# Optimization experiments

Hardware: AMD Instinct MI355X
Metric: run time of the kernel (lower is better)

The kernel has to match this reference:

```python
import jax, jax.numpy as jnp
import numpy as np

NEG = jnp.float32(-1e30)  # log-space -inf surrogate (safe for grads)


def _ctc_neg_log_likelihood(logprobs, labels, input_lens, label_lens):
    """CTC forward (alpha) recursion, blank=0.
    logprobs: (T, N, V) log-softmax outputs; labels: (N, L) int; lens: (N,).
    Returns per-sample negative log-likelihood (N,).
    """
    T, N, V = logprobs.shape
    L = labels.shape[1]
    S = 2 * L + 1
    # Extended label sequence: blank, l1, blank, l2, ..., blank
    z = jnp.zeros((N, S), dtype=labels.dtype).at[:, 1::2].set(labels)
    # Per-step emission log-probs for extended labels: (T, N, S)
    lp = logprobs[:, jnp.arange(N)[:, None], z]
    # Skip connection s-2 -> s allowed iff z[s] != blank and z[s] != z[s-2]
    z_m2 = jnp.pad(z, ((0, 0), (2, 0)))[:, :S]
    skip = (z != 0) & (z != z_m2)
    skip = skip.at[:, :2].set(False)

    alpha0 = jnp.full((N, S), NEG, dtype=logprobs.dtype)
    alpha0 = alpha0.at[:, 0].set(lp[0, :, 0]).at[:, 1].set(lp[0, :, 1])

    def step(alpha, xs):
        lp_t, t = xs
        a1 = jnp.pad(alpha, ((0, 0), (1, 0)), constant_values=NEG)[:, :S]
        a2 = jnp.pad(alpha, ((0, 0), (2, 0)), constant_values=NEG)[:, :S]
        a2 = jnp.where(skip, a2, NEG)
        new = jnp.logaddexp(jnp.logaddexp(alpha, a1), a2) + lp_t
        # Freeze alpha once past each sample's input length
        new = jnp.where((t < input_lens)[:, None], new, alpha)
        return new, None

    ts = jnp.arange(1, T)
    alpha, _ = jax.lax.scan(step, alpha0, (lp[1:], ts))

    idx_blank = (2 * label_lens).astype(jnp.int32)  # final blank position
    end1 = jnp.take_along_axis(alpha, idx_blank[:, None], axis=1)[:, 0]
    end2 = jnp.take_along_axis(alpha, (idx_blank - 1)[:, None], axis=1)[:, 0]
    return -jnp.logaddexp(end1, end2)


def setup_inputs() -> dict:
    key = jax.random.key(0)
    k1, k2, k3, k4, k5 = jax.random.split(key, 5)
    N, T, D, V, L = 16, 512, 512, 4096, 128
    encoder_out = jax.random.normal(k1, (N, T, D), dtype=jnp.float32)
    W = jax.random.normal(k2, (D, V), dtype=jnp.float32) / jnp.sqrt(jnp.float32(D))
    b = jnp.zeros((V,), dtype=jnp.float32)
    encoder_out_lens = jax.random.randint(k3, (N,), 300, T + 1, dtype=jnp.int32)
    padded_labels = jax.random.randint(k4, (N, L), 1, V, dtype=jnp.int32)
    label_lengths = jax.random.randint(k5, (N,), 64, L + 1, dtype=jnp.int32)
    return {
        "encoder_out": encoder_out,
        "W": W,
        "b": b,
        "encoder_out_lens": encoder_out_lens,
        "padded_labels": padded_labels,
        "label_lengths": label_lengths,
    }


def reference(encoder_out, W, b, encoder_out_lens, padded_labels, label_lengths):
    # Dropout is identity in eval mode. proj -> (N, T, V)
    logits = jnp.einsum("ntd,dv->ntv", encoder_out, W) + b
    # transpose(0,1).log_softmax(2) -> (T, N, V)
    logprobs = jax.nn.log_softmax(logits.transpose(1, 0, 2), axis=2)
    nll = _ctc_neg_log_likelihood(logprobs, padded_labels, encoder_out_lens, label_lengths)
    # reduction='sum', then divided by batch size
    return jnp.sum(nll) / padded_labels.shape[0]
```

## Files before the change

### kernel.cpp

```cpp
#include <hip/hip_runtime.h>

#define NEGF (-1e30f)
#define LOG2E 1.4426950408889634f
#define LN2d  0.6931471805599453

typedef __attribute__((ext_vector_type(8))) short bf16x8;
typedef __attribute__((ext_vector_type(4))) float f32x4;

__device__ __forceinline__ unsigned short f2bf(float x) {
  unsigned u = __float_as_uint(x);
  unsigned r = (u + 0x7FFFu + ((u >> 16) & 1u)) >> 16;
  return (unsigned short)r;
}


__device__ __forceinline__ void d_cvtx(int bid, int tid,
                                       const float* __restrict__ X,
                                       unsigned short* __restrict__ Xbf) {
  const int i = bid * 256 + tid;
  float4 v = ((const float4*)X)[i];
  ushort4 h;
  h.x = f2bf(v.x); h.y = f2bf(v.y); h.z = f2bf(v.z); h.w = f2bf(v.w);
  ((ushort4*)Xbf)[i] = h;
}

__device__ __forceinline__ void d_gather(int bid, int tid,
                                         const float* __restrict__ W,
                                         const float* __restrict__ b,
                                         const int* __restrict__ labels,
                                         float* __restrict__ Wgt,
                                         float* __restrict__ gb) {
  const int n  = bid >> 7;
  const int kc = bid & 127;
  const int k0 = kc << 2;
  for (int idx = tid; idx < 4 * 129; idx += 256) {
    const int kk = idx / 129;
    const int j  = idx - kk * 129;
    const int c  = (j == 0) ? 0 : labels[n * 128 + (j - 1)];
    const int k  = k0 + kk;
    Wgt[((size_t)(n * 512 + k)) * 132 + j] = W[(size_t)k * 4096 + c];
    if (kc == 0 && kk == 0) gb[n * 129 + j] = b[c];
  }
}

__device__ __forceinline__ void d_glp_raw(int bid, int tid, char* smem,
                                          const float* __restrict__ X,
                                          const float* __restrict__ Wgt,
                                          const float* __restrict__ gb,
                                          const int* __restrict__ lens,
                                          float* __restrict__ g) {
  const int n  = bid >> 4;
  const int t0 = (bid & 15) << 5;
  if (t0 >= lens[n]) return;
  const int m0 = n * 512 + t0;
  float (*xs)[512] = (float (*)[512])smem;
  {
    const float4* Xv = (const float4*)(X + (size_t)m0 * 512);
    float4* xsv = (float4*)(&xs[0][0]);
    for (int i = tid; i < 32 * 128; i += 256) xsv[i] = Xv[i];
  }
  __syncthreads();
  const int j = tid;
  if (j >= 129) return;
  const float* wp = Wgt + (size_t)(n * 512) * 132 + j;
  float acc[32];
#pragma unroll
  for (int r = 0; r < 32; ++r) acc[r] = 0.f;
  float w0 = wp[0], w1 = wp[132], w2 = wp[264], w3 = wp[396];
  for (int k4 = 0; k4 < 128; ++k4) {
    const int kn = (k4 + 1) & 127;
    float p0 = wp[(size_t)(kn * 4 + 0) * 132];
    float p1 = wp[(size_t)(kn * 4 + 1) * 132];
    float p2 = wp[(size_t)(kn * 4 + 2) * 132];
    float p3 = wp[(size_t)(kn * 4 + 3) * 132];
#pragma unroll
    for (int r = 0; r < 32; ++r) {
      float4 x4 = *(const float4*)(&xs[r][k4 << 2]);
      acc[r] = fmaf(x4.x, w0, acc[r]);
      acc[r] = fmaf(x4.y, w1, acc[r]);
      acc[r] = fmaf(x4.z, w2, acc[r]);
      acc[r] = fmaf(x4.w, w3, acc[r]);
    }
    w0 = p0; w1 = p1; w2 = p2; w3 = p3;
  }
  const float bb = gb[n * 129 + j];
#pragma unroll
  for (int r = 0; r < 32; ++r)
    g[(size_t)(m0 + r) * 132 + j] = (acc[r] + bb) * LOG2E;
}

__device__ __forceinline__ void d_wtrans(int bid, int tid, char* smem,
                                         const float* __restrict__ W,
                                         unsigned short* __restrict__ Wt) {
  float (*tile)[65] = (float (*)[65])smem;
  const int kb = bid & 7;
  const int vb = bid >> 3;
  const int k0 = kb << 6, v0 = vb << 6;
#pragma unroll
  for (int it = 0; it < 16; ++it) {
    const int idx = it * 256 + tid;
    const int r = idx >> 6, c = idx & 63;
    tile[r][c] = W[(size_t)(k0 + r) * 4096 + v0 + c];
  }
  __syncthreads();
#pragma unroll
  for (int it = 0; it < 16; ++it) {
    const int idx = it * 256 + tid;
    const int vr = idx >> 6, kc = idx & 63;
    Wt[(size_t)(v0 + vr) * 512 + k0 + kc] = f2bf(tile[kc][vr]);
  }
}

__device__ __forceinline__ void stage_tile(const unsigned short* __restrict__ src,
                                           int r0, char* ldsbase, int wave,
                                           int tid, int kbyte) {
#pragma unroll
  for (int j = 0; j < 2; ++j) {
    const int chunk = (tid & 3) ^ ((tid >> 3) & 3);
    const char* gp = (const char*)src +
        (size_t)(r0 + j * 64 + (tid >> 2)) * 1024 + kbyte + chunk * 16;
    char* lp = ldsbase + j * 4096 + wave * 1024;
    __builtin_amdgcn_global_load_lds(
        (const __attribute__((address_space(1))) unsigned int*)gp,
        (__attribute__((address_space(3))) unsigned int*)lp, 16, 0, 0);
  }
}

__device__ __forceinline__ void d_gemm(int gid, int tid, char* smem,
                                       const unsigned short* __restrict__ Xbf,
                                       const unsigned short* __restrict__ Wt,
                                       const float* __restrict__ bvec,
                                       const int* __restrict__ lens,
                                       float* __restrict__ pg) {
  const int bm = gid >> 5;
  const int bn = gid & 31;
  const int n  = bm >> 2;
  const int t0 = (bm & 3) << 7;
  if (t0 >= lens[n]) return;
  const int m0 = bm << 7;
  const int v0 = bn << 7;

  const int wave = tid >> 6;
  const int lane = tid & 63;
  const int lrow = lane & 15;
  const int lk   = (lane >> 4) * 16;
  const int lks  = lk ^ (((lrow >> 1) & 3) << 4);
  const int wr   = wave >> 1;
  const int wn   = wave & 1;

  f32x4 acc[4][4];
#pragma unroll
  for (int mi = 0; mi < 4; ++mi)
#pragma unroll
    for (int ni = 0; ni < 4; ++ni) acc[mi][ni] = (f32x4){0.f, 0.f, 0.f, 0.f};

  {
    char* buf = smem;
    stage_tile(Xbf, m0, buf + 0,    wave, tid, 0);
    stage_tile(Wt,  v0, buf + 8192, wave, tid, 0);
  }
  __syncthreads();

  int cur = 0;
  for (int kk = 0; kk < 16; ++kk) {
    if (kk < 15) {
      char* nbuf = smem + (cur ^ 1) * 16384;
      const int kb = (kk + 1) << 6;
      stage_tile(Xbf, m0, nbuf + 0,    wave, tid, kb);
      stage_tile(Wt,  v0, nbuf + 8192, wave, tid, kb);
    }
    const char* buf = smem + cur * 16384;
    bf16x8 ah[4], bh[4];
#pragma unroll
    for (int mi = 0; mi < 4; ++mi) {
      const int off = (wr * 64 + mi * 16 + lrow) * 64 + lks;
      ah[mi] = *(const bf16x8*)(buf + off);
    }
#pragma unroll
    for (int ni = 0; ni < 4; ++ni) {
      const int off = (wn * 64 + ni * 16 + lrow) * 64 + lks;
      bh[ni] = *(const bf16x8*)(buf + 8192 + off);
    }
#pragma unroll
    for (int mi = 0; mi < 4; ++mi)
#pragma unroll
      for (int ni = 0; ni < 4; ++ni)
        acc[mi][ni] = __builtin_amdgcn_mfma_f32_16x16x32_bf16(ah[mi], bh[ni], acc[mi][ni], 0, 0, 0);
    __syncthreads();
    cur ^= 1;
  }

  const float lg2e = LOG2E;
  float bias[4];
#pragma unroll
  for (int ni = 0; ni < 4; ++ni) bias[ni] = bvec[v0 + wn * 64 + ni * 16 + lrow];
  float* part = (float*)(smem + 32768);
#pragma unroll
  for (int mi = 0; mi < 4; ++mi)
#pragma unroll
    for (int reg = 0; reg < 4; ++reg) {
      float s = 0.f;
#pragma unroll
      for (int ni = 0; ni < 4; ++ni)
        s += exp2f((acc[mi][ni][reg] + bias[ni]) * lg2e);
#pragma unroll
      for (int msk = 1; msk < 16; msk <<= 1) s += __shfl_xor(s, msk);
      if (lrow == 0)
        part[(wr * 64 + mi * 16 + (lane >> 4) * 4 + reg) * 2 + wn] = s;
    }
  __syncthreads();
  if (tid < 128)
    pg[(size_t)(m0 + tid) * 32 + bn] = part[tid * 2 + 0] + part[tid * 2 + 1];
}

__device__ __forceinline__ float lae32(float x, float y, float z) {
  float m = fmaxf(fmaxf(x, y), z);
  float e = exp2f(x - m) + exp2f(y - m) + exp2f(z - m);
  return m + __log2f(e);
}

__device__ __forceinline__ float lae3n(float x, float y, float z) {
  float m = fmaxf(fmaxf(x, y), z);
  float e = __expf(x - m) + __expf(y - m) + __expf(z - m);
  return m + __logf(e);
}

__device__ __forceinline__ void stage32(const float* __restrict__ gsrc,
                                        char* ldsbase, int tid, int wave) {
#pragma unroll
  for (int k = 0; k < 4; ++k) {
    const char* gp = (const char*)gsrc + k * 4096 + (size_t)tid * 16;
    char* lp = ldsbase + k * 4096 + wave * 1024;
    __builtin_amdgcn_global_load_lds(
        (const __attribute__((address_space(1))) unsigned int*)gp,
        (__attribute__((address_space(3))) unsigned int*)lp, 16, 0, 0);
  }
  if (tid < 32) {
    const char* gp = (const char*)gsrc + 16384 + (size_t)tid * 16;
    char* lp = ldsbase + 16384;
    __builtin_amdgcn_global_load_lds(
        (const __attribute__((address_space(1))) unsigned int*)gp,
        (__attribute__((address_space(3))) unsigned int*)lp, 16, 0, 0);
  }
}

__device__ void d_scan(int sbid, int tid, char* smem,
                       const float* __restrict__ g,
                       const int* __restrict__ labels,
                       const int* __restrict__ in_lens,
                       const int* __restrict__ lab_lens,
                       float* __restrict__ af,
                       float* __restrict__ ab) {
  const int n    = sbid >> 1;
  const int dir  = sbid & 1;
  const int wave = tid >> 6;
  const int l    = tid & 63;
  const int len  = in_lens[n];
  const int tm   = len >> 1;
  const float* gn = g + (size_t)n * 512 * 132;
  const int s0 = 5 * l;

  int jm0, jm1, jm2, jm3, jm4;
  {
    int jmv[5];
#pragma unroll
    for (int i = 0; i < 5; ++i) {
      const int s = s0 + i;
      jmv[i] = (s < 257 && (s & 1)) ? ((s + 1) >> 1) : 0;
    }
    jm0 = jmv[0]; jm1 = jmv[1]; jm2 = jmv[2]; jm3 = jmv[3]; jm4 = jmv[4];
  }

  if (dir == 0) {
    bool sk0, sk1, sk2, sk3, sk4;
    {
      bool skv[5];
#pragma unroll
      for (int i = 0; i < 5; ++i) {
        const int s = s0 + i;
        skv[i] = false;
        if (s < 257 && (s & 1) && s >= 3) {
          const int li = (s - 1) >> 1;
          const int cl = labels[n * 128 + li];
          skv[i] = (cl != 0) && (cl != labels[n * 128 + li - 1]);
        }
      }
      sk0 = skv[0]; sk1 = skv[1]; sk2 = skv[2]; sk3 = skv[3]; sk4 = skv[4];
    }
    stage32(gn, smem, tid, wave);
    __syncthreads();

    float a0 = NEGF, a1 = NEGF, a2 = NEGF, a3 = NEGF, a4 = NEGF;
    if (tid < 64 && l == 0) {
      const float* B0 = (const float*)smem;
      a0 = B0[0]; a1 = B0[1];
    }
    float a3p = NEGF, a4p = NEGF;

    int t = 1, c = 0;
    while (true) {
      const bool more = ((c + 1) << 5) <= tm;
      if (more)
        stage32(gn + (size_t)((c + 1) << 5) * 132,
                smem + ((c + 1) & 1) * 16896, tid, wave);
      if (tid < 64) {
        const float* B = (const float*)(smem + (c & 1) * 16896);
        const int ce = (c << 5) + 31;
        const int tend = (tm < ce) ? tm : ce;
        int ro = (t - (c << 5)) * 132;
        float p0 = B[ro + jm0], p1 = B[ro + jm1], p2 = B[ro + jm2],
              p3 = B[ro + jm3], p4 = B[ro + jm4];
        for (; t <= tend; ++t) {
          const int ro2 = (t < tend) ? ro + 132 : ro;
          const float q0 = B[ro2 + jm0];
          const float q1 = B[ro2 + jm1];
          const float q2 = B[ro2 + jm2];
          const float q3 = B[ro2 + jm3];
          const float q4 = B[ro2 + jm4];
          float x3 = a3p, x4 = a4p;
          if (l == 0) { x3 = NEGF; x4 = NEGF; }
          const float n3 = lae32(a3, a2, sk3 ? a1 : NEGF) + p3;
          const float n4 = lae32(a4, a3, sk4 ? a2 : NEGF) + p4;
          a3p = __shfl_up(n3, 1);
          a4p = __shfl_up(n4, 1);
          const float n0 = lae32(a0, x4, sk0 ? x3 : NEGF) + p0;
          const float n1 = lae32(a1, a0, sk1 ? x4 : NEGF) + p1;
          const float n2 = lae32(a2, a1, sk2 ? a0 : NEGF) + p2;
          a0 = n0; a1 = n1; a2 = n2; a3 = n3; a4 = n4;
          p0 = q0; p1 = q1; p2 = q2; p3 = q3; p4 = q4;
          ro = ro2;
        }
      }
      if (!more) break;
      __syncthreads();
      ++c;
    }
    if (tid < 64) {
      float* o = af + n * 320 + s0;
      o[0] = a0; o[1] = a1; o[2] = a2; o[3] = a3; o[4] = a4;
    }
  } else {
    bool skd0, skd1, skd2, skd3, skd4;
    {
      bool skv[5];
#pragma unroll
      for (int i = 0; i < 5; ++i) {
        const int s2 = s0 + i + 2;
        skv[i] = false;
        if (s2 < 257 && (s2 & 1) && s2 >= 3) {
          const int li = (s2 - 1) >> 1;
          const int cl = labels[n * 128 + li];
          skv[i] = (cl != 0) && (cl != labels[n * 128 + li - 1]);
        }
      }
      skd0 = skv[0]; skd1 = skv[1]; skd2 = skv[2]; skd3 = skv[3]; skd4 = skv[4];
    }
    int c = (len - 1) >> 5;
    stage32(gn + (size_t)(c << 5) * 132, smem + (c & 1) * 16896, tid, wave);
    __syncthreads();

    float b0, b1, b2, b3, b4;
    {
      const int ll = lab_lens[n];
      const int i1 = 2 * ll, i2 = 2 * ll - 1;
      b0 = (s0 + 0 == i1 || s0 + 0 == i2) ? 0.f : NEGF;
      b1 = (s0 + 1 == i1 || s0 + 1 == i2) ? 0.f : NEGF;
      b2 = (s0 + 2 == i1 || s0 + 2 == i2) ? 0.f : NEGF;
      b3 = (s0 + 3 == i1 || s0 + 3 == i2) ? 0.f : NEGF;
      b4 = (s0 + 4 == i1 || s0 + 4 == i2) ? 0.f : NEGF;
    }

    int t = len - 2;
    while (true) {
      const bool more = (c << 5) > tm + 1;
      if (more)
        stage32(gn + (size_t)((c - 1) << 5) * 132,
                smem + ((c - 1) & 1) * 16896, tid, wave);
      if (tid < 64) {
        const float* B = (const float*)(smem + (c & 1) * 16896);
        const int cl0 = (c << 5) - 1;
        const int tlo = (tm > cl0) ? tm : cl0;
        int ro = (t + 1 - (c << 5)) * 132;
        float p0 = B[ro + jm0], p1 = B[ro + jm1], p2 = B[ro + jm2],
              p3 = B[ro + jm3], p4 = B[ro + jm4];
        for (; t >= tlo; --t) {
          const int ro2 = (t - 1 >= tlo) ? ro - 132 : ro;
          const float q0 = B[ro2 + jm0];
          const float q1 = B[ro2 + jm1];
          const float q2 = B[ro2 + jm2];
          const float q3 = B[ro2 + jm3];
          const float q4 = B[ro2 + jm4];
          const float c0 = b0 + p0;
          const float c1 = b1 + p1;
          float c5 = __shfl_down(c0, 1);
          float c6 = __shfl_down(c1, 1);
          const float c2 = b2 + p2;
          const float c3 = b3 + p3;
          const float c4 = b4 + p4;
          const float m0n = lae32(c0, c1, skd0 ? c2 : NEGF);
          const float m1n = lae32(c1, c2, skd1 ? c3 : NEGF);
          const float m2n = lae32(c2, c3, skd2 ? c4 : NEGF);
          if (l == 63) { c5 = NEGF; c6 = NEGF; }
          const float m3n = lae32(c3, c4, skd3 ? c5 : NEGF);
          const float m4n = lae32(c4, c5, skd4 ? c6 : NEGF);
          b0 = m0n; b1 = m1n; b2 = m2n; b3 = m3n; b4 = m4n;
          p0 = q0; p1 = q1; p2 = q2; p3 = q3; p4 = q4;
          ro = ro2;
        }
      }
      if (!more) break;
      __syncthreads();
      --c;
    }
    if (tid < 64) {
      float* o = ab + n * 320 + s0;
      o[0] = b0; o[1] = b1; o[2] = b2; o[3] = b3; o[4] = b4;
    }
  }
}


__global__ __launch_bounds__(256) void k_prep1(const float* __restrict__ X,
                                               unsigned short* __restrict__ Xbf,
                                               const float* __restrict__ W,
                                               const float* __restrict__ b,
                                               const int* __restrict__ labels,
                                               float* __restrict__ Wgt,
                                               float* __restrict__ gb) {
  const int bid = blockIdx.x;
  if (bid < 4096) d_cvtx(bid, threadIdx.x, X, Xbf);
  else            d_gather(bid - 4096, threadIdx.x, W, b, labels, Wgt, gb);
}

__global__ __launch_bounds__(256) void k_prep2(const float* __restrict__ X,
                                               const float* __restrict__ Wgt,
                                               const float* __restrict__ gb,
                                               const int* __restrict__ lens,
                                               float* __restrict__ g,
                                               const float* __restrict__ W,
                                               unsigned short* __restrict__ Wt) {
  __shared__ __align__(16) char smem[65536];
  const int bid = blockIdx.x;
  if (bid < 256) d_glp_raw(bid, threadIdx.x, smem, X, Wgt, gb, lens, g);
  else           d_wtrans(bid - 256, threadIdx.x, smem, W, Wt);
}

__global__ __launch_bounds__(256, 4) void k_main(const float* __restrict__ g,
                                                 const int* __restrict__ labels,
                                                 const int* __restrict__ in_lens,
                                                 const int* __restrict__ lab_lens,
                                                 float* __restrict__ af,
                                                 float* __restrict__ ab,
                                                 const unsigned short* __restrict__ Xbf,
                                                 const unsigned short* __restrict__ Wt,
                                                 const float* __restrict__ bvec,
                                                 float* __restrict__ pg) {
  __shared__ __align__(16) char smem[33792];
  const int bid = blockIdx.x;
  if (bid < 32) {
    __builtin_amdgcn_s_setprio(1);
    d_scan(bid, threadIdx.x, smem, g, labels, in_lens, lab_lens, af, ab);
    __builtin_amdgcn_s_setprio(0);
  } else {
    d_gemm(bid - 32, threadIdx.x, smem, Xbf, Wt, bvec, in_lens, pg);
  }
}

__global__ __launch_bounds__(256) void k_tail(const float* __restrict__ pg,
                                              const int* __restrict__ lens,
                                              const float* __restrict__ af,
                                              const float* __restrict__ ab,
                                              float* __restrict__ nll) {
  const int n = blockIdx.x, tid = threadIdx.x;
  const int len = lens[n];
  __shared__ double red[256];
  double s = 0.0;
  for (int t = tid; t < len; t += 256) {
    const float4* p = (const float4*)(pg + ((size_t)(n * 512 + t)) * 32);
    float e = 0.f;
#pragma unroll
    for (int i = 0; i < 8; ++i) { float4 v = p[i]; e += v.x + v.y + v.z + v.w; }
    s += (double)__logf(e);
  }
  red[tid] = s;
  __syncthreads();
  for (int off = 128; off > 0; off >>= 1) {
    if (tid < off) red[tid] += red[tid + off];
    __syncthreads();
  }
  if (tid < 64) {
    const int l = tid;
    const int s0 = 5 * l;
    float v0 = NEGF, v1 = NEGF, v2 = NEGF, v3 = NEGF, v4 = NEGF;
    const float* f = af + n * 320 + s0;
    const float* bb = ab + n * 320 + s0;
    if (s0 + 0 < 257) v0 = f[0] + bb[0];
    if (s0 + 1 < 257) v1 = f[1] + bb[1];
    if (s0 + 2 < 257) v2 = f[2] + bb[2];
    if (s0 + 3 < 257) v3 = f[3] + bb[3];
    if (s0 + 4 < 257) v4 = f[4] + bb[4];
    float M = fmaxf(fmaxf(v0, v1), fmaxf(fmaxf(v2, v3), v4));
#pragma unroll
    for (int off = 1; off < 64; off <<= 1) M = fmaxf(M, __shfl_xor(M, off));
    float e = exp2f(v0 - M) + exp2f(v1 - M) + exp2f(v2 - M)
            + exp2f(v3 - M) + exp2f(v4 - M);
#pragma unroll
    for (int off = 1; off < 64; off <<= 1) e += __shfl_xor(e, off);
    if (l == 0)
      nll[n] = (float)(red[0] - (double)(M + __log2f(e)) * LN2d);
  }
}

__global__ void k_finish(const float* __restrict__ nll, float* __restrict__ out) {
  const int l = threadIdx.x;
  float v = (l < 16) ? nll[l] : 0.f;
#pragma unroll
  for (int off = 8; off > 0; off >>= 1) v += __shfl_down(v, off);
  if (l == 0) out[0] = v * 0.0625f;
}

__global__ void k_gather_w(const float* __restrict__ W,
                           const float* __restrict__ b,
                           const int* __restrict__ labels,
                           float* __restrict__ Wgt,
                           float* __restrict__ gb) {
  d_gather(blockIdx.x, threadIdx.x, W, b, labels, Wgt, gb);
}

__global__ __launch_bounds__(256) void k_glp(const float* __restrict__ X,
                                             const float* __restrict__ Wgt,
                                             const float* __restrict__ gb,
                                             const float* __restrict__ lse,
                                             const int* __restrict__ lens,
                                             float* __restrict__ g) {
  const int blk = blockIdx.x;
  const int n   = blk >> 4;
  const int t0  = (blk & 15) << 5;
  if (t0 >= lens[n]) return;
  const int m0 = n * 512 + t0;
  __shared__ float xs[32][512];
  {
    const float4* Xv = (const float4*)(X + (size_t)m0 * 512);
    float4* xsv = (float4*)(&xs[0][0]);
    for (int i = threadIdx.x; i < 32 * 128; i += 256) xsv[i] = Xv[i];
  }
  __syncthreads();
  const int j = threadIdx.x;
  if (j >= 129) return;
  const float* wp = Wgt + (size_t)(n * 512) * 132 + j;
  float acc[32];
#pragma unroll
  for (int r = 0; r < 32; ++r) acc[r] = 0.f;
  float w0 = wp[0], w1 = wp[132], w2 = wp[264], w3 = wp[396];
  for (int k4 = 0; k4 < 128; ++k4) {
    const int kn = (k4 + 1) & 127;
    float p0 = wp[(size_t)(kn * 4 + 0) * 132];
    float p1 = wp[(size_t)(kn * 4 + 1) * 132];
    float p2 = wp[(size_t)(kn * 4 + 2) * 132];
    float p3 = wp[(size_t)(kn * 4 + 3) * 132];
#pragma unroll
    for (int r = 0; r < 32; ++r) {
      float4 x4 = *(const float4*)(&xs[r][k4 << 2]);
      acc[r] = fmaf(x4.x, w0, acc[r]);
      acc[r] = fmaf(x4.y, w1, acc[r]);
      acc[r] = fmaf(x4.z, w2, acc[r]);
      acc[r] = fmaf(x4.w, w3, acc[r]);
    }
    w0 = p0; w1 = p1; w2 = p2; w3 = p3;
  }
  const float bb = gb[n * 129 + j];
#pragma unroll
  for (int r = 0; r < 32; ++r)
    g[(size_t)(m0 + r) * 132 + j] = acc[r] + bb - lse[m0 + r];
}

__global__ void k_ctc_g(const float* __restrict__ g,
                        const int* __restrict__ labels,
                        const int* __restrict__ in_lens,
                        const int* __restrict__ lab_lens,
                        float* __restrict__ nll) {
  const int n = blockIdx.x;
  const int l = threadIdx.x;
  const float* gn = g + (size_t)n * 512 * 132;
  const int len = in_lens[n];
  const int s0 = 5 * l;
  int jm[5]; bool sk[5];
#pragma unroll
  for (int i = 0; i < 5; ++i) {
    const int s = s0 + i;
    const bool valid = (s < 257);
    jm[i] = (valid && (s & 1)) ? ((s + 1) >> 1) : 0;
    sk[i] = false;
    if (valid && (s & 1) && s >= 3) {
      const int li = (s - 1) >> 1;
      const int cl = labels[n * 128 + li];
      sk[i] = (cl != 0) && (cl != labels[n * 128 + li - 1]);
    }
  }
  float a[5];
  a[0] = (l == 0) ? gn[0] : NEGF;
  a[1] = (l == 0) ? gn[1] : NEGF;
  a[2] = NEGF; a[3] = NEGF; a[4] = NEGF;
  float lp[5];
#pragma unroll
  for (int i = 0; i < 5; ++i) lp[i] = gn[132 + jm[i]];
  for (int t = 1; t < len; ++t) {
    const int tp = (t + 1 < len) ? (t + 1) : t;
    float np[5];
#pragma unroll
    for (int i = 0; i < 5; ++i) np[i] = gn[(size_t)tp * 132 + jm[i]];
    float a3p = __shfl_up(a[3], 1);
    float a4p = __shfl_up(a[4], 1);
    if (l == 0) { a3p = NEGF; a4p = NEGF; }
    const float b0 = lae3n(a[0], a4p,  sk[0] ? a3p  : NEGF) + lp[0];
    const float b1 = lae3n(a[1], a[0], sk[1] ? a4p  : NEGF) + lp[1];
    const float b2 = lae3n(a[2], a[1], sk[2] ? a[0] : NEGF) + lp[2];
    const float b3 = lae3n(a[3], a[2], sk[3] ? a[1] : NEGF) + lp[3];
    const float b4 = lae3n(a[4], a[3], sk[4] ? a[2] : NEGF) + lp[4];
    a[0] = b0; a[1] = b1; a[2] = b2; a[3] = b3; a[4] = b4;
#pragma unroll
    for (int i = 0; i < 5; ++i) lp[i] = np[i];
  }
  __shared__ float al[320];
#pragma unroll
  for (int i = 0; i < 5; ++i) al[s0 + i] = a[i];
  __syncthreads();
  if (l == 0) {
    const int ll  = lab_lens[n];
    const int idx = 2 * ll;
    const float e1 = al[idx], e2 = al[idx - 1];
    const float m = fmaxf(e1, e2);
    const float r = m + __logf(__expf(e1 - m) + __expf(e2 - m));
    nll[n] = -r;
  }
}

__global__ __launch_bounds__(512, 2) void k_lse(const float* __restrict__ X,
                                                const float* __restrict__ W,
                                                const float* __restrict__ b,
                                                const int* __restrict__ lens,
                                                float* __restrict__ lse,
                                                float* __restrict__ red_g) {
  const int blk = blockIdx.x;
  const int n   = blk >> 4;
  const int t0  = (blk & 15) << 5;
  if (t0 >= lens[n]) return;
  const int m0 = n * 512 + t0;
  __shared__ float xs[32][512];
  {
    const float4* Xv = (const float4*)(X + (size_t)m0 * 512);
    float4* xsv = (float4*)(&xs[0][0]);
    for (int i = threadIdx.x; i < 32 * 128; i += 512) xsv[i] = Xv[i];
  }
  float* redb = red_g + (size_t)blk * 256;
  for (int i = threadIdx.x; i < 256; i += 512) redb[i] = 0.f;
  __syncthreads();
  const int wave = threadIdx.x >> 6;
  const int lane = threadIdx.x & 63;
  for (int j = 0; j < 4; ++j) {
    const int v = (j << 10) + (threadIdx.x << 1);
    const float* Wv = W + v;
    float2 acc[32];
#pragma unroll
    for (int r = 0; r < 32; ++r) acc[r] = make_float2(0.f, 0.f);
    float2 w0 = *(const float2*)(Wv + 0 * 4096);
    float2 w1 = *(const float2*)(Wv + 1 * 4096);
    float2 w2 = *(const float2*)(Wv + 2 * 4096);
    float2 w3 = *(const float2*)(Wv + 3 * 4096);
    for (int k4 = 0; k4 < 128; ++k4) {
      const int kn = (k4 + 1) & 127;
      float2 p0 = *(const float2*)(Wv + (kn * 4 + 0) * 4096);
      float2 p1 = *(const float2*)(Wv + (kn * 4 + 1) * 4096);
      float2 p2 = *(const float2*)(Wv + (kn * 4 + 2) * 4096);
      float2 p3 = *(const float2*)(Wv + (kn * 4 + 3) * 4096);
#pragma unroll
      for (int r = 0; r < 32; ++r) {
        float4 x4 = *(const float4*)(&xs[r][k4 << 2]);
        acc[r].x = fmaf(x4.x, w0.x, acc[r].x);
        acc[r].y = fmaf(x4.x, w0.y, acc[r].y);
        acc[r].x = fmaf(x4.y, w1.x, acc[r].x);
        acc[r].y = fmaf(x4.y, w1.y, acc[r].y);
        acc[r].x = fmaf(x4.z, w2.x, acc[r].x);
        acc[r].y = fmaf(x4.z, w2.y, acc[r].y);
        acc[r].x = fmaf(x4.w, w3.x, acc[r].x);
        acc[r].y = fmaf(x4.w, w3.y, acc[r].y);
      }
      w0 = p0; w1 = p1; w2 = p2; w3 = p3;
    }
    const float2 bb = *(const float2*)(b + v);
#pragma unroll
    for (int r = 0; r < 32; ++r) {
      float e = __expf(acc[r].x + bb.x) + __expf(acc[r].y + bb.y);
#pragma unroll
      for (int off = 32; off > 0; off >>= 1) e += __shfl_xor(e, off);
      if (lane == 0) redb[wave * 32 + r] += e;
    }
  }
  __syncthreads();
  if (threadIdx.x < 32) {
    float s = 0.f;
#pragma unroll
    for (int w = 0; w < 8; ++w) s += redb[w * 32 + threadIdx.x];
    lse[m0 + threadIdx.x] = __logf(s);
  }
}

extern "C" void kernel_launch(void* const* d_in, const int* in_sizes, int n_in,
                              void* d_out, int out_size, void* d_ws, size_t ws_size,
                              hipStream_t stream) {
  const float* X        = (const float*)d_in[0];
  const float* W        = (const float*)d_in[1];
  const float* b        = (const float*)d_in[2];
  const int*   in_lens  = (const int*)d_in[3];
  const int*   labels   = (const int*)d_in[4];
  const int*   lab_lens = (const int*)d_in[5];
  float* out = (float*)d_out;
  char* wsb = (char*)d_ws;

  const size_t NEED = 34906240;
  if (ws_size >= NEED) {
    float* pg  = (float*)(wsb + 32768);
    float* Wgt = (float*)(wsb + 1081344);
    float* gb  = (float*)(wsb + 5406720);
    float* g   = (float*)(wsb + 5414976);
    float* nll = (float*)(wsb + 9740352);
    unsigned short* Xbf = (unsigned short*)(wsb + 9740416);
    unsigned short* Wt  = (unsigned short*)(wsb + 18129024);
    float* af = (float*)(wsb + 26517632);
    float* ab = (float*)(wsb + 26517632 + 20480);

    k_prep1<<<dim3(6144), dim3(256), 0, stream>>>(X, Xbf, W, b, labels, Wgt, gb);
    k_prep2<<<dim3(768), dim3(256), 0, stream>>>(X, Wgt, gb, in_lens, g, W, Wt);
    k_main<<<dim3(2080), dim3(256), 0, stream>>>(g, labels, in_lens, lab_lens,
                                                 af, ab, Xbf, Wt, b, pg);
    k_tail<<<dim3(16), dim3(256), 0, stream>>>(pg, in_lens, af, ab, nll);
    k_finish<<<dim3(1), dim3(64), 0, stream>>>(nll, out);
  } else {
    float* ws    = (float*)d_ws;
    float* lse   = ws;
    float* red_g = ws + 8192;
    float* Wgt   = ws + 8192 + 65536;
    float* gb    = Wgt + 1081344;
    float* g     = gb + 2064;
    float* nll   = g + 1081344;
    k_lse<<<dim3(256), dim3(512), 0, stream>>>(X, W, b, in_lens, lse, red_g);
    k_gather_w<<<dim3(2048), dim3(256), 0, stream>>>(W, b, labels, Wgt, gb);
    k_glp<<<dim3(256), dim3(256), 0, stream>>>(X, Wgt, gb, lse, in_lens, g);
    k_ctc_g<<<dim3(16), dim3(64), 0, stream>>>(g, labels, in_lens, lab_lens, nll);
    k_finish<<<dim3(1), dim3(64), 0, stream>>>(nll, out);
  }
}
```

Before: 186.7 us.

## Move W transpose into prep1 and split label-logit GEMM into 8-row blocks

The W transpose to bf16 moves out of the second prep kernel and into the first, so it runs alongside the X conversion and the label gather. The gathered-label logit GEMM becomes a standalone kernel with 8-row tiles (1024 blocks) instead of 32-row tiles (256 blocks). The smaller tiles use less shared memory and fewer accumulator registers, raising occupancy and parallelism, at the cost of re-reading the gathered weights four times as often. It also removes the s_setprio boost on the CTC scan blocks in the main kernel, which could delay the scan on the critical path.

```diff
diff --git a/kernel.cpp b/kernel.cpp
--- a/kernel.cpp
+++ b/kernel.cpp
@@ -41,52 +41,6 @@
     Wgt[((size_t)(n * 512 + k)) * 132 + j] = W[(size_t)k * 4096 + c];
     if (kc == 0 && kk == 0) gb[n * 129 + j] = b[c];
   }
-}
-
-__device__ __forceinline__ void d_glp_raw(int bid, int tid, char* smem,
-                                          const float* __restrict__ X,
-                                          const float* __restrict__ Wgt,
-                                          const float* __restrict__ gb,
-                                          const int* __restrict__ lens,
-                                          float* __restrict__ g) {
-  const int n  = bid >> 4;
-  const int t0 = (bid & 15) << 5;
-  if (t0 >= lens[n]) return;
-  const int m0 = n * 512 + t0;
-  float (*xs)[512] = (float (*)[512])smem;
-  {
-    const float4* Xv = (const float4*)(X + (size_t)m0 * 512);
-    float4* xsv = (float4*)(&xs[0][0]);
-    for (int i = tid; i < 32 * 128; i += 256) xsv[i] = Xv[i];
-  }
-  __syncthreads();
-  const int j = tid;
-  if (j >= 129) return;
-  const float* wp = Wgt + (size_t)(n * 512) * 132 + j;
-  float acc[32];
-#pragma unroll
-  for (int r = 0; r < 32; ++r) acc[r] = 0.f;
-  float w0 = wp[0], w1 = wp[132], w2 = wp[264], w3 = wp[396];
-  for (int k4 = 0; k4 < 128; ++k4) {
-    const int kn = (k4 + 1) & 127;
-    float p0 = wp[(size_t)(kn * 4 + 0) * 132];
-    float p1 = wp[(size_t)(kn * 4 + 1) * 132];
-    float p2 = wp[(size_t)(kn * 4 + 2) * 132];
-    float p3 = wp[(size_t)(kn * 4 + 3) * 132];
-#pragma unroll
-    for (int r = 0; r < 32; ++r) {
-      float4 x4 = *(const float4*)(&xs[r][k4 << 2]);
-      acc[r] = fmaf(x4.x, w0, acc[r]);
-      acc[r] = fmaf(x4.y, w1, acc[r]);
-      acc[r] = fmaf(x4.z, w2, acc[r]);
-      acc[r] = fmaf(x4.w, w3, acc[r]);
-    }
-    w0 = p0; w1 = p1; w2 = p2; w3 = p3;
-  }
-  const float bb = gb[n * 129 + j];
-#pragma unroll
-  for (int r = 0; r < 32; ++r)
-    g[(size_t)(m0 + r) * 132 + j] = (acc[r] + bb) * LOG2E;
 }
 
 __device__ __forceinline__ void d_wtrans(int bid, int tid, char* smem,
@@ -426,23 +380,59 @@
                                                const float* __restrict__ b,
                                                const int* __restrict__ labels,
                                                float* __restrict__ Wgt,
-                                               float* __restrict__ gb) {
+                                               float* __restrict__ gb,
+                                               unsigned short* __restrict__ Wt) {
+  __shared__ __align__(16) char smem[16640];
   const int bid = blockIdx.x;
-  if (bid < 4096) d_cvtx(bid, threadIdx.x, X, Xbf);
-  else            d_gather(bid - 4096, threadIdx.x, W, b, labels, Wgt, gb);
-}
-
-__global__ __launch_bounds__(256) void k_prep2(const float* __restrict__ X,
-                                               const float* __restrict__ Wgt,
-                                               const float* __restrict__ gb,
-                                               const int* __restrict__ lens,
-                                               float* __restrict__ g,
-                                               const float* __restrict__ W,
-                                               unsigned short* __restrict__ Wt) {
-  __shared__ __align__(16) char smem[65536];
+  if (bid < 4096)      d_cvtx(bid, threadIdx.x, X, Xbf);
+  else if (bid < 6144) d_gather(bid - 4096, threadIdx.x, W, b, labels, Wgt, gb);
+  else                 d_wtrans(bid - 6144, threadIdx.x, smem, W, Wt);
+}
+
+__global__ __launch_bounds__(256) void k_glp8(const float* __restrict__ X,
+                                              const float* __restrict__ Wgt,
+                                              const float* __restrict__ gb,
+                                              const int* __restrict__ lens,
+                                              float* __restrict__ g) {
+  __shared__ float xs[8][512];
   const int bid = blockIdx.x;
-  if (bid < 256) d_glp_raw(bid, threadIdx.x, smem, X, Wgt, gb, lens, g);
-  else           d_wtrans(bid - 256, threadIdx.x, smem, W, Wt);
+  const int n  = bid >> 6;
+  const int r0 = (bid & 63) << 3;
+  if (r0 >= lens[n]) return;
+  const int m0 = n * 512 + r0;
+  {
+    const float4* Xv = (const float4*)(X + (size_t)m0 * 512);
+    float4* xsv = (float4*)(&xs[0][0]);
+    for (int i = threadIdx.x; i < 8 * 128; i += 256) xsv[i] = Xv[i];
+  }
+  __syncthreads();
+  const int j = threadIdx.x;
+  if (j >= 129) return;
+  const float* wp = Wgt + (size_t)(n * 512) * 132 + j;
+  float acc[8];
+#pragma unroll
+  for (int r = 0; r < 8; ++r) acc[r] = 0.f;
+  float w0 = wp[0], w1 = wp[132], w2 = wp[264], w3 = wp[396];
+  for (int k4 = 0; k4 < 128; ++k4) {
+    const int kn = (k4 + 1) & 127;
+    float p0 = wp[(size_t)(kn * 4 + 0) * 132];
+    float p1 = wp[(size_t)(kn * 4 + 1) * 132];
+    float p2 = wp[(size_t)(kn * 4 + 2) * 132];
+    float p3 = wp[(size_t)(kn * 4 + 3) * 132];
+#pragma unroll
+    for (int r = 0; r < 8; ++r) {
+      float4 x4 = *(const float4*)(&xs[r][k4 << 2]);
+      acc[r] = fmaf(x4.x, w0, acc[r]);
+      acc[r] = fmaf(x4.y, w1, acc[r]);
+      acc[r] = fmaf(x4.z, w2, acc[r]);
+      acc[r] = fmaf(x4.w, w3, acc[r]);
+    }
+    w0 = p0; w1 = p1; w2 = p2; w3 = p3;
+  }
+  const float bb = gb[n * 129 + j];
+#pragma unroll
+  for (int r = 0; r < 8; ++r)
+    g[(size_t)(m0 + r) * 132 + j] = (acc[r] + bb) * LOG2E;
 }
 
 __global__ __launch_bounds__(256, 4) void k_main(const float* __restrict__ g,
@@ -458,9 +448,7 @@
   __shared__ __align__(16) char smem[33792];
   const int bid = blockIdx.x;
   if (bid < 32) {
-    __builtin_amdgcn_s_setprio(1);
     d_scan(bid, threadIdx.x, smem, g, labels, in_lens, lab_lens, af, ab);
-    __builtin_amdgcn_s_setprio(0);
   } else {
     d_gemm(bid - 32, threadIdx.x, smem, Xbf, Wt, bvec, in_lens, pg);
   }
@@ -729,8 +717,8 @@
     float* af = (float*)(wsb + 26517632);
     float* ab = (float*)(wsb + 26517632 + 20480);
 
-    k_prep1<<<dim3(6144), dim3(256), 0, stream>>>(X, Xbf, W, b, labels, Wgt, gb);
-    k_prep2<<<dim3(768), dim3(256), 0, stream>>>(X, Wgt, gb, in_lens, g, W, Wt);
+    k_prep1<<<dim3(6656), dim3(256), 0, stream>>>(X, Xbf, W, b, labels, Wgt, gb, Wt);
+    k_glp8<<<dim3(1024), dim3(256), 0, stream>>>(X, Wgt, gb, in_lens, g);
     k_main<<<dim3(2080), dim3(256), 0, stream>>>(g, labels, in_lens, lab_lens,
                                                  af, ab, Xbf, Wt, b, pg);
     k_tail<<<dim3(16), dim3(256), 0, stream>>>(pg, in_lens, af, ab, nll);
```

Result: faster. 168.9 us, median of 2 (-9.5%).
